# Optimization experiments

Measured on AMD Instinct MI355X. Metric: run time of the kernel, lower is better.

The kernel has to match this reference:

```python
import jax, jax.numpy as jnp
import numpy as np

EPS = 1e-8
NUM_HEADS = 8


def _conv(x, w, pad_h, pad_w):
    # x: (B,C,H,W) NCHW; w: (O,I,kh,kw) OIHW
    return jax.lax.conv_general_dilated(
        x, w, window_strides=(1, 1),
        padding=((pad_h, pad_h), (pad_w, pad_w)),
        dimension_numbers=('NCHW', 'OIHW', 'NCHW'))


def _mc_layernorm(x, g, b):
    # normalize over the features axis (axis=2) with per-(channel,feature) affine
    mu = jnp.mean(x, axis=2, keepdims=True)
    var = jnp.var(x, axis=2, keepdims=True)
    xn = (x - mu) * jax.lax.rsqrt(var + EPS)
    return xn * g[None, :, :, None] + b[None, :, :, None]


def _mc_attention(x, mem, wq, wk, wv, wo, prev_qk):
    # x: (B,C,F,W); projections are Conv2d with kernel (1,3), padding (0,1)
    B, _, F, W = x.shape
    q = _conv(x, wq, 0, 1)
    k = _conv(mem, wk, 0, 1)
    v = _conv(mem, wv, 0, 1)
    OC = q.shape[1]
    d = F // NUM_HEADS

    def split(t):  # (B,OC,F,W) -> (B,OC,heads,W,d)
        return t.reshape(B, OC, NUM_HEADS, d, W).transpose(0, 1, 2, 4, 3)

    q, k, v = split(q), split(k), split(v)
    qk = jnp.einsum('bchqd,bchkd->bchqk', q, k) / jnp.sqrt(jnp.asarray(d, x.dtype))
    if prev_qk is not None:
        qk = qk + prev_qk  # cross-layer additive qk bias accumulation
    a = jnp.einsum('bchqk,bchkd->bchqd', jax.nn.softmax(qk, axis=-1), v)
    a = a.transpose(0, 1, 2, 4, 3).reshape(B, OC, F, W)
    return _conv(a, wo, 0, 1), qk


def setup_inputs() -> dict:
    key = jax.random.key(0)
    ks = jax.random.split(key, 24)
    B, C, OC, F, W, H, EXP = 1, 8, 8, 1024, 512, NUM_HEADS, 4
    s = lambda fan: 1.0 / np.sqrt(fan)
    inp = {
        'x': jax.random.normal(ks[0], (B, C, F, W), jnp.float32),
        'skip': jax.random.normal(ks[1], (B, C, F, W), jnp.float32),
        'prev_qk1': jax.random.normal(ks[2], (B, OC, H, W, W), jnp.float32) * 0.5,
        'prev_qk2': jax.random.normal(ks[3], (B, OC, H, W, W), jnp.float32) * 0.5,
        'skip_qk': jax.random.normal(ks[4], (B, OC, H, W, W), jnp.float32) * 0.5,
        # norm1 / attn1 (self-attention on C channels -> OC)
        'g1': jnp.ones((C, F), jnp.float32),
        'b1': jnp.zeros((C, F), jnp.float32),
        'wq1': jax.random.normal(ks[5], (OC, C, 1, 3), jnp.float32) * s(C * 3),
        'wk1': jax.random.normal(ks[6], (OC, C, 1, 3), jnp.float32) * s(C * 3),
        'wv1': jax.random.normal(ks[7], (OC, C, 1, 3), jnp.float32) * s(C * 3),
        'wo1': jax.random.normal(ks[8], (OC, OC, 1, 3), jnp.float32) * s(OC * 3),
        # norm2 / attn2 (query from C+OC channels, memory = skip with C channels)
        'g2': jnp.ones((C + OC, F), jnp.float32),
        'b2': jnp.zeros((C + OC, F), jnp.float32),
        'wq2': jax.random.normal(ks[9], (OC, C + OC, 1, 3), jnp.float32) * s((C + OC) * 3),
        'wk2': jax.random.normal(ks[10], (OC, C, 1, 3), jnp.float32) * s(C * 3),
        'wv2': jax.random.normal(ks[11], (OC, C, 1, 3), jnp.float32) * s(C * 3),
        'wo2': jax.random.normal(ks[12], (OC, OC, 1, 3), jnp.float32) * s(OC * 3),
        # norm3 / conv MLP
        'g3': jnp.ones((C + 2 * OC, F), jnp.float32),
        'b3': jnp.zeros((C + 2 * OC, F), jnp.float32),
        'wc1': jax.random.normal(ks[13], (C * EXP, C + 2 * OC, 3, 3), jnp.float32) * s((C + 2 * OC) * 9),
        'wc2': jax.random.normal(ks[14], (C, C * EXP, 3, 3), jnp.float32) * s(C * EXP * 9),
    }
    return inp


def reference(x, skip, prev_qk1, prev_qk2, skip_qk,
              g1, b1, wq1, wk1, wv1, wo1,
              g2, b2, wq2, wk2, wv2, wo2,
              g3, b3, wc1, wc2):
    pq1 = prev_qk1 + skip_qk
    nx = _mc_layernorm(x, g1, b1)
    z, pq1 = _mc_attention(nx, nx, wq1, wk1, wv1, wo1, pq1)
    h = jnp.concatenate([x, z], axis=1)
    pq2 = skip_qk + pq1 + prev_qk2
    nh = _mc_layernorm(h, g2, b2)
    z, pq2 = _mc_attention(nh, skip, wq2, wk2, wv2, wo2, pq2)
    h = jnp.concatenate([h, z], axis=1)
    t = _conv(_mc_layernorm(h, g3, b3), wc1, 1, 1)
    t = jnp.square(jax.nn.relu(t))  # SquaredReLU
    z = _conv(t, wc2, 1, 1)
    # dropout is identity in eval mode
    return (x + z, pq1, pq2)
```

## Files before the change

kernel.cpp:

```cpp
#include <hip/hip_runtime.h>
#include <hip/hip_bf16.h>

#define F    1024
#define WW   512
#define DH   128
#define NPAIR 64
#define PW   514
#define PF   1026

using short8  = __attribute__((ext_vector_type(8))) short;
using short4v = __attribute__((ext_vector_type(4))) short;
using float4v = __attribute__((ext_vector_type(4))) float;

__device__ __forceinline__ float bf2f(unsigned short u) {
    union { unsigned int i; float f; } x; x.i = ((unsigned int)u) << 16; return x.f;
}
__device__ __forceinline__ unsigned short f2bf(float f) {
    union { float f; unsigned int i; } x; x.f = f;
    unsigned int r = x.i + 0x7fff + ((x.i >> 16) & 1);
    return (unsigned short)(r >> 16);
}

__global__ __launch_bounds__(256) void k_ln(
    const float* __restrict__ s0, const float* __restrict__ s1,
    const float* __restrict__ s2,
    const float* __restrict__ g, const float* __restrict__ b,
    unsigned short* __restrict__ out)
{
    int c  = blockIdx.x >> 5;
    int w0 = (blockIdx.x & 31) << 4;
    const float* src = (c < 8) ? s0 : (c < 16) ? s1 : s2;
    src += (size_t)(c & 7) * F * WW;
    int tx = threadIdx.x & 15, ty = threadIdx.x >> 4;

    float sum = 0.f, ssq = 0.f;
    for (int f = ty; f < F; f += 16) {
        float v = src[f * WW + w0 + tx];
        sum += v; ssq += v * v;
    }
    __shared__ float sm[16][17], sq[16][17];
    __shared__ float mu_s[16], rs_s[16];
    sm[ty][tx] = sum; sq[ty][tx] = ssq;
    __syncthreads();
    if (threadIdx.x < 16) {
        float s = 0.f, q = 0.f;
        #pragma unroll
        for (int i = 0; i < 16; i++) { s += sm[i][threadIdx.x]; q += sq[i][threadIdx.x]; }
        float mu  = s * (1.f / F);
        float var = q * (1.f / F) - mu * mu;
        mu_s[threadIdx.x] = mu;
        rs_s[threadIdx.x] = rsqrtf(var + 1e-8f);
    }
    __syncthreads();
    float mu = mu_s[tx], rs = rs_s[tx];
    unsigned short* o = out + (size_t)c * F * WW;
    for (int f = ty; f < F; f += 16) {
        float v = src[f * WW + w0 + tx];
        float r = (v - mu) * rs * g[c * F + f] + b[c * F + f];
        o[f * WW + w0 + tx] = f2bf(r);
    }
}

__global__ __launch_bounds__(256) void k_ln3_stats(
    const float* __restrict__ s0, const float* __restrict__ s1,
    const float* __restrict__ s2,
    float* __restrict__ mu3, float* __restrict__ rs3)
{
    int c  = blockIdx.x >> 5;
    int w0 = (blockIdx.x & 31) << 4;
    const float* src = (c < 8) ? s0 : (c < 16) ? s1 : s2;
    src += (size_t)(c & 7) * F * WW;
    int tx = threadIdx.x & 15, ty = threadIdx.x >> 4;

    float sum = 0.f, ssq = 0.f;
    for (int f = ty; f < F; f += 16) {
        float v = src[f * WW + w0 + tx];
        sum += v; ssq += v * v;
    }
    __shared__ float sm[16][17], sq[16][17];
    sm[ty][tx] = sum; sq[ty][tx] = ssq;
    __syncthreads();
    if (threadIdx.x < 16) {
        float s = 0.f, q = 0.f;
        #pragma unroll
        for (int i = 0; i < 16; i++) { s += sm[i][threadIdx.x]; q += sq[i][threadIdx.x]; }
        float mu  = s * (1.f / F);
        float var = q * (1.f / F) - mu * mu;
        mu3[c * WW + w0 + threadIdx.x] = mu;
        rs3[c * WW + w0 + threadIdx.x] = rsqrtf(var + 1e-8f);
    }
}

__global__ __launch_bounds__(256) void k_ln3_apply(
    const float* __restrict__ s0, const float* __restrict__ s1,
    const float* __restrict__ s2,
    const float* __restrict__ mu3, const float* __restrict__ rs3,
    const float* __restrict__ g, const float* __restrict__ b,
    unsigned short* __restrict__ outp)
{
    int p = blockIdx.x * 256 + threadIdx.x;
    int f = p >> 9, w = p & 511;
    unsigned short buf[32];
    #pragma unroll
    for (int c = 0; c < 24; c++) {
        const float* src = (c < 8) ? s0 : (c < 16) ? s1 : s2;
        float v = src[((size_t)(c & 7) * F + f) * WW + w];
        float r = (v - mu3[c * WW + w]) * rs3[c * WW + w] * g[c * F + f] + b[c * F + f];
        buf[c] = f2bf(r);
    }
    #pragma unroll
    for (int c = 24; c < 32; c++) buf[c] = 0;
    unsigned short* op = outp + ((size_t)(f + 1) * PW + (w + 1)) * 32;
    #pragma unroll
    for (int q = 0; q < 4; q++) *(short8*)(op + q * 8) = *(const short8*)(buf + q * 8);
}

__global__ void k_pad(unsigned short* __restrict__ a, unsigned short* __restrict__ b)
{
    int i = blockIdx.x * 256 + threadIdx.x;
    if (i >= 3076) return;
    int f, w;
    if (i < 514)       { f = 0;    w = i; }
    else if (i < 1028) { f = 1025; w = i - 514; }
    else { int j = i - 1028; f = 1 + (j >> 1); w = (j & 1) ? 513 : 0; }
    size_t off = ((size_t)f * PW + w) * 32;
    short8 z = {};
    #pragma unroll
    for (int q = 0; q < 4; q++) {
        *(short8*)(a + off + q * 8) = z;
        *(short8*)(b + off + q * 8) = z;
    }
}

__global__ void k_prep(const float* __restrict__ wc1, const float* __restrict__ wc2,
                       unsigned short* __restrict__ A1, unsigned short* __restrict__ A2)
{
    int i = blockIdx.x * 256 + threadIdx.x;
    if (i < 9216) {
        int ic = i & 31, row = i >> 5;
        int o16 = row & 15, tm = row >> 4;
        int tap = tm >> 1, m = tm & 1;
        int oc = m * 16 + o16;
        A1[i] = (ic < 24) ? f2bf(wc1[(oc * 24 + ic) * 9 + tap]) : (unsigned short)0;
    }
    if (i < 4608) {
        int ic = i & 31, row = i >> 5;
        int o = row & 15, tap = row >> 4;
        A2[i] = (o < 8) ? f2bf(wc2[(o * 32 + ic) * 9 + tap]) : (unsigned short)0;
    }
}

__global__ __launch_bounds__(256) void k_conv1m(
    const unsigned short* __restrict__ inp, const unsigned short* __restrict__ A1,
    unsigned short* __restrict__ outp)
{
    int wv = threadIdx.x >> 6, lane = threadIdx.x & 63;
    int lr = lane & 15, lkg = lane >> 4;

    short8 a[9][2];
    #pragma unroll
    for (int tap = 0; tap < 9; tap++)
        #pragma unroll
        for (int m = 0; m < 2; m++)
            a[tap][m] = *(const short8*)(A1 + ((tap * 2 + m) * 16 + lr) * 32 + lkg * 8);

    int f = blockIdx.x >> 1;
    int half = blockIdx.x & 1;
    for (int it = 0; it < 4; it++) {
        int w0 = (half * 16 + wv * 4 + it) * 16;
        float4v acc0 = {}, acc1 = {};
        #pragma unroll
        for (int dy = 0; dy < 3; dy++)
            #pragma unroll
            for (int dx = 0; dx < 3; dx++) {
                short8 bfrag = *(const short8*)(inp +
                    ((size_t)(f + dy) * PW + (w0 + lr + dx)) * 32 + lkg * 8);
                acc0 = __builtin_amdgcn_mfma_f32_16x16x32_bf16(a[dy*3+dx][0], bfrag, acc0, 0, 0, 0);
                acc1 = __builtin_amdgcn_mfma_f32_16x16x32_bf16(a[dy*3+dx][1], bfrag, acc1, 0, 0, 0);
            }
        unsigned short* op = outp + ((size_t)(f + 1) * PW + (w0 + lr + 1)) * 32;
        short4v o0, o1;
        #pragma unroll
        for (int r = 0; r < 4; r++) {
            float v0 = fmaxf(acc0[r], 0.f);
            float v1 = fmaxf(acc1[r], 0.f);
            o0[r] = (short)f2bf(v0 * v0);
            o1[r] = (short)f2bf(v1 * v1);
        }
        *(short4v*)(op + lkg * 4)      = o0;
        *(short4v*)(op + 16 + lkg * 4) = o1;
    }
}

__global__ __launch_bounds__(256) void k_conv2m(
    const unsigned short* __restrict__ inp, const unsigned short* __restrict__ A2,
    const float* __restrict__ x, float* __restrict__ out)
{
    int wv = threadIdx.x >> 6, lane = threadIdx.x & 63;
    int lr = lane & 15, lkg = lane >> 4;

    short8 a[9];
    #pragma unroll
    for (int tap = 0; tap < 9; tap++)
        a[tap] = *(const short8*)(A2 + (tap * 16 + lr) * 32 + lkg * 8);

    int f = blockIdx.x >> 1;
    int half = blockIdx.x & 1;
    for (int it = 0; it < 4; it++) {
        int w0 = (half * 16 + wv * 4 + it) * 16;
        float4v acc = {};
        #pragma unroll
        for (int dy = 0; dy < 3; dy++)
            #pragma unroll
            for (int dx = 0; dx < 3; dx++) {
                short8 bfrag = *(const short8*)(inp +
                    ((size_t)(f + dy) * PW + (w0 + lr + dx)) * 32 + lkg * 8);
                acc = __builtin_amdgcn_mfma_f32_16x16x32_bf16(a[dy*3+dx], bfrag, acc, 0, 0, 0);
            }
        if (lkg < 2) {
            #pragma unroll
            for (int r = 0; r < 4; r++) {
                int oc = lkg * 4 + r;
                size_t off = ((size_t)oc * F + f) * WW + w0 + lr;
                out[off] = x[off] + acc[r];
            }
        }
    }
}

__global__ __launch_bounds__(256) void k_qkv(
    const unsigned short* __restrict__ srcQ, int CinQ, const float* __restrict__ wq,
    const void* __restrict__ srcKV, int kvBf16,
    const float* __restrict__ wk, const float* __restrict__ wv,
    unsigned short* __restrict__ qT, unsigned short* __restrict__ kT,
    unsigned short* __restrict__ v)
{
    int vb = ((blockIdx.x & 31) << 4) + (blockIdx.x >> 5);
    int p0 = (vb * 256 + threadIdx.x) * 4;
    int f  = p0 >> 9;
    int w0 = p0 & 511;
    int h = f >> 7, jf = f & 127;

    float accq[8][4];
    #pragma unroll
    for (int o = 0; o < 8; o++) { accq[o][0]=0.f; accq[o][1]=0.f; accq[o][2]=0.f; accq[o][3]=0.f; }
    for (int ic = 0; ic < CinQ; ic++) {
        const unsigned short* s = srcQ + ((size_t)ic * F + f) * WW;
        float val[6];
        #pragma unroll
        for (int i = 0; i < 6; i++) {
            int w = w0 - 1 + i;
            val[i] = (w >= 0 && w < WW) ? bf2f(s[w]) : 0.f;
        }
        #pragma unroll
        for (int o = 0; o < 8; o++)
            #pragma unroll
            for (int t = 0; t < 3; t++) {
                float wt = wq[(o * CinQ + ic) * 3 + t];
                #pragma unroll
                for (int p = 0; p < 4; p++) accq[o][p] = fmaf(wt, val[p + t], accq[o][p]);
            }
    }
    #pragma unroll
    for (int o = 0; o < 8; o++)
        #pragma unroll
        for (int p = 0; p < 4; p++)
            qT[((size_t)(o * 8 + h) * WW + w0 + p) * DH + jf] = f2bf(accq[o][p]);

    float acck[8][4], accv[8][4];
    #pragma unroll
    for (int o = 0; o < 8; o++)
        #pragma unroll
        for (int p = 0; p < 4; p++) { acck[o][p] = 0.f; accv[o][p] = 0.f; }
    for (int ic = 0; ic < 8; ic++) {
        float val[6];
        if (kvBf16) {
            const unsigned short* s = (const unsigned short*)srcKV + ((size_t)ic * F + f) * WW;
            #pragma unroll
            for (int i = 0; i < 6; i++) {
                int w = w0 - 1 + i;
                val[i] = (w >= 0 && w < WW) ? bf2f(s[w]) : 0.f;
            }
        } else {
            const float* s = (const float*)srcKV + ((size_t)ic * F + f) * WW;
            #pragma unroll
            for (int i = 0; i < 6; i++) {
                int w = w0 - 1 + i;
                val[i] = (w >= 0 && w < WW) ? s[w] : 0.f;
            }
        }
        #pragma unroll
        for (int o = 0; o < 8; o++)
            #pragma unroll
            for (int t = 0; t < 3; t++) {
                float wtk = wk[(o * 8 + ic) * 3 + t];
                float wtv = wv[(o * 8 + ic) * 3 + t];
                #pragma unroll
                for (int p = 0; p < 4; p++) {
                    acck[o][p] = fmaf(wtk, val[p + t], acck[o][p]);
                    accv[o][p] = fmaf(wtv, val[p + t], accv[o][p]);
                }
            }
    }
    #pragma unroll
    for (int o = 0; o < 8; o++) {
        #pragma unroll
        for (int p = 0; p < 4; p++)
            kT[((size_t)(o * 8 + h) * WW + w0 + p) * DH + jf] = f2bf(acck[o][p]);
        short4v pv;
        #pragma unroll
        for (int p = 0; p < 4; p++) pv[p] = (short)f2bf(accv[o][p]);
        *(short4v*)(v + ((size_t)o * F + f) * WW + w0) = pv;
    }
}

__global__ __launch_bounds__(256) void k_attn(
    const unsigned short* __restrict__ qT, const unsigned short* __restrict__ kT,
    const unsigned short* __restrict__ v,
    const float* __restrict__ a0, const float* __restrict__ a1,
    const float* __restrict__ a2, int nsrc,
    float* __restrict__ pq, unsigned short* __restrict__ aout)
{
    int pair = blockIdx.x & 63;
    int qw0  = (blockIdx.x >> 6) << 6;

    __shared__ unsigned short Ks[64 * 136];
    __shared__ unsigned short Vt[128 * 72];
    __shared__ unsigned short P [64 * 72];

    int tid = threadIdx.x;
    const unsigned short* qb = qT + ((size_t)pair * WW + qw0) * DH;
    const unsigned short* kb = kT + (size_t)pair * WW * DH;
    const unsigned short* vb = v  + (size_t)pair * DH * WW;

    int wv = tid >> 6, lane = tid & 63;
    int lr = lane & 15, lkg = lane >> 4;
    int qrow = qw0 + wv * 16 + lr;

    short8 bq[4];
    #pragma unroll
    for (int dk = 0; dk < 4; dk++)
        bq[dk] = *(const short8*)(qb + (size_t)(wv * 16 + lr) * DH + dk * 32 + lkg * 8);

    float4v acc[8] = {};
    float mrun = -1e30f, lrun = 0.f;
    const float scale = 0.08838834764831845f;
    size_t bbase = (size_t)pair * WW * WW + (size_t)qrow * WW;

    for (int kc = 0; kc < 8; kc++) {
        __syncthreads();

        float4v b0v[4], b1v[4], b2v[4];
        #pragma unroll
        for (int mi = 0; mi < 4; mi++)
            b0v[mi] = *(const float4v*)(a0 + bbase + kc * 64 + mi * 16 + lkg * 4);
        if (nsrc > 1) {
            #pragma unroll
            for (int mi = 0; mi < 4; mi++)
                b1v[mi] = *(const float4v*)(a1 + bbase + kc * 64 + mi * 16 + lkg * 4);
        }
        if (nsrc > 2) {
            #pragma unroll
            for (int mi = 0; mi < 4; mi++)
                b2v[mi] = *(const float4v*)(a2 + bbase + kc * 64 + mi * 16 + lkg * 4);
        }

        #pragma unroll
        for (int it = 0; it < 4; it++) {
            int idx = it * 256 + tid;
            int r = idx >> 4, c = idx & 15;
            *(short8*)(Ks + r * 136 + c * 8) =
                *(const short8*)(kb + (size_t)(kc * 64 + r) * DH + c * 8);
        }
        #pragma unroll
        for (int it = 0; it < 4; it++) {
            int idx = it * 256 + tid;
            int j = idx >> 3, c = idx & 7;
            *(short8*)(Vt + j * 72 + c * 8) =
                *(const short8*)(vb + (size_t)j * WW + kc * 64 + c * 8);
        }
        __syncthreads();

        float4v sacc[4] = {};
        #pragma unroll
        for (int dk = 0; dk < 4; dk++) {
            short8 ak[4];
            #pragma unroll
            for (int mi = 0; mi < 4; mi++)
                ak[mi] = *(const short8*)(Ks + (mi * 16 + lr) * 136 + dk * 32 + lkg * 8);
            #pragma unroll
            for (int mi = 0; mi < 4; mi++)
                sacc[mi] = __builtin_amdgcn_mfma_f32_16x16x32_bf16(ak[mi], bq[dk], sacc[mi], 0, 0, 0);
        }

        float sv[4][4];
        float mx = -1e30f;
        #pragma unroll
        for (int mi = 0; mi < 4; mi++) {
            int k0 = kc * 64 + mi * 16 + lkg * 4;
            float4v s;
            #pragma unroll
            for (int r = 0; r < 4; r++) s[r] = sacc[mi][r] * scale + b0v[mi][r];
            if (nsrc > 1) {
                #pragma unroll
                for (int r = 0; r < 4; r++) s[r] += b1v[mi][r];
            }
            if (nsrc > 2) {
                #pragma unroll
                for (int r = 0; r < 4; r++) s[r] += b2v[mi][r];
            }
            *(float4v*)(pq + bbase + k0) = s;
            #pragma unroll
            for (int r = 0; r < 4; r++) { sv[mi][r] = s[r]; mx = fmaxf(mx, s[r]); }
        }
        mx = fmaxf(mx, __shfl_xor(mx, 16));
        mx = fmaxf(mx, __shfl_xor(mx, 32));
        float mnew  = fmaxf(mrun, mx);
        float alpha = __expf(mrun - mnew);
        float lsum  = 0.f;
        #pragma unroll
        for (int mi = 0; mi < 4; mi++) {
            short4v pk;
            #pragma unroll
            for (int r = 0; r < 4; r++) {
                float e = __expf(sv[mi][r] - mnew);
                lsum += e;
                pk[r] = (short)f2bf(e);
            }
            *(short4v*)(P + (wv * 16 + lr) * 72 + mi * 16 + lkg * 4) = pk;
        }
        lsum += __shfl_xor(lsum, 16);
        lsum += __shfl_xor(lsum, 32);
        lrun = lrun * alpha + lsum;
        mrun = mnew;

        #pragma unroll
        for (int mt = 0; mt < 8; mt++)
            #pragma unroll
            for (int r = 0; r < 4; r++) acc[mt][r] *= alpha;

        #pragma unroll
        for (int ks = 0; ks < 2; ks++) {
            short8 bp = *(const short8*)(P + (wv * 16 + lr) * 72 + ks * 32 + lkg * 8);
            #pragma unroll
            for (int mt = 0; mt < 8; mt++) {
                short8 av = *(const short8*)(Vt + (mt * 16 + lr) * 72 + ks * 32 + lkg * 8);
                acc[mt] = __builtin_amdgcn_mfma_f32_16x16x32_bf16(av, bp, acc[mt], 0, 0, 0);
            }
        }
    }

    float linv = 1.f / lrun;
    unsigned short* ab = aout + (size_t)pair * DH * WW + qw0 + wv * 16 + lr;
    #pragma unroll
    for (int mt = 0; mt < 8; mt++)
        #pragma unroll
        for (int r = 0; r < 4; r++) {
            int d = mt * 16 + lkg * 4 + r;
            ab[(size_t)d * WW] = f2bf(acc[mt][r] * linv);
        }
}

__global__ __launch_bounds__(256) void k_wo(
    const unsigned short* __restrict__ a, const float* __restrict__ w,
    float* __restrict__ z)
{
    int p0 = (blockIdx.x * 256 + threadIdx.x) * 4;
    int f = p0 >> 9, w0 = p0 & 511;
    float acc[8][4];
    #pragma unroll
    for (int o = 0; o < 8; o++)
        #pragma unroll
        for (int p = 0; p < 4; p++) acc[o][p] = 0.f;
    for (int ic = 0; ic < 8; ic++) {
        const unsigned short* s = a + ((size_t)ic * F + f) * WW;
        float val[6];
        #pragma unroll
        for (int i = 0; i < 6; i++) {
            int ww = w0 - 1 + i;
            val[i] = (ww >= 0 && ww < WW) ? bf2f(s[ww]) : 0.f;
        }
        #pragma unroll
        for (int o = 0; o < 8; o++)
            #pragma unroll
            for (int t = 0; t < 3; t++) {
                float wt = w[(o * 8 + ic) * 3 + t];
                #pragma unroll
                for (int p = 0; p < 4; p++) acc[o][p] = fmaf(wt, val[p + t], acc[o][p]);
            }
    }
    #pragma unroll
    for (int o = 0; o < 8; o++) {
        float4v ov;
        #pragma unroll
        for (int p = 0; p < 4; p++) ov[p] = acc[o][p];
        *(float4v*)(z + ((size_t)o * F + f) * WW + w0) = ov;
    }
}

extern "C" void kernel_launch(void* const* d_in, const int* in_sizes, int n_in,
                              void* d_out, int out_size, void* d_ws, size_t ws_size,
                              hipStream_t stream) {
    const float* x        = (const float*)d_in[0];
    const float* skip     = (const float*)d_in[1];
    const float* prev_qk1 = (const float*)d_in[2];
    const float* prev_qk2 = (const float*)d_in[3];
    const float* skip_qk  = (const float*)d_in[4];
    const float* g1  = (const float*)d_in[5];
    const float* b1  = (const float*)d_in[6];
    const float* wq1 = (const float*)d_in[7];
    const float* wk1 = (const float*)d_in[8];
    const float* wv1 = (const float*)d_in[9];
    const float* wo1 = (const float*)d_in[10];
    const float* g2  = (const float*)d_in[11];
    const float* b2  = (const float*)d_in[12];
    const float* wq2 = (const float*)d_in[13];
    const float* wk2 = (const float*)d_in[14];
    const float* wv2 = (const float*)d_in[15];
    const float* wo2 = (const float*)d_in[16];
    const float* g3  = (const float*)d_in[17];
    const float* b3  = (const float*)d_in[18];
    const float* wc1 = (const float*)d_in[19];
    const float* wc2 = (const float*)d_in[20];

    char* ws = (char*)d_ws;
    float*          z1 = (float*)(ws + 0);
    float*          z2 = (float*)(ws + 16777216);
    unsigned short* qT = (unsigned short*)(ws + 33554432);
    unsigned short* kT = (unsigned short*)(ws + 41943040);
    unsigned short* vB = (unsigned short*)(ws + 50331648);
    unsigned short* nh = (unsigned short*)(ws + 58720256);
    unsigned short* aB = (unsigned short*)(ws + 75497472);
    unsigned short* nh3p = (unsigned short*)(ws + 33554432);
    unsigned short* tBp  = (unsigned short*)(ws + 67305728);
    unsigned short* A1p  = (unsigned short*)(ws + 101057024);
    unsigned short* A2p  = (unsigned short*)(ws + 101075456);
    float*          mu3  = (float*)(ws + 101084672);
    float*          rs3  = (float*)(ws + 101133824);

    float* out0 = (float*)d_out;
    float* pq1  = out0 + 4194304;
    float* pq2  = pq1 + 16777216;

    k_prep<<<36, 256, 0, stream>>>(wc1, wc2, A1p, A2p);

    k_ln  <<<8 * 32,  256, 0, stream>>>(x, nullptr, nullptr, g1, b1, nh);
    k_qkv <<<512,     256, 0, stream>>>(nh, 8, wq1, nh, 1, wk1, wv1, qT, kT, vB);
    k_attn<<<512,     256, 0, stream>>>(qT, kT, vB, prev_qk1, skip_qk, nullptr, 2, pq1, aB);
    k_wo  <<<512,     256, 0, stream>>>(aB, wo1, z1);

    k_ln  <<<16 * 32, 256, 0, stream>>>(x, z1, nullptr, g2, b2, nh);
    k_qkv <<<512,     256, 0, stream>>>(nh, 16, wq2, skip, 0, wk2, wv2, qT, kT, vB);
    k_attn<<<512,     256, 0, stream>>>(qT, kT, vB, skip_qk, pq1, prev_qk2, 3, pq2, aB);
    k_wo  <<<512,     256, 0, stream>>>(aB, wo2, z2);

    k_pad      <<<13,      256, 0, stream>>>(nh3p, tBp);
    k_ln3_stats<<<24 * 32, 256, 0, stream>>>(x, z1, z2, mu3, rs3);
    k_ln3_apply<<<2048,    256, 0, stream>>>(x, z1, z2, mu3, rs3, g3, b3, nh3p);
    k_conv1m   <<<2048,    256, 0, stream>>>(nh3p, A1p, tBp);
    k_conv2m   <<<2048,    256, 0, stream>>>(tBp, A2p, x, out0);
}
```

Measured before the change: 771.1 us.

## Stage Q/K transposes through LDS and prefetch K/V tiles in registers in attention

In k_qkv the blocks are retiled into 32x32 (f,w) tiles and the transposed Q and K outputs are staged through a shared-memory buffer. This turns scattered 2-byte stores into contiguous 16-byte stores. In k_attn the next K/V chunk is loaded into registers while the current chunk is being computed, with setprio around the MFMA sections and a launch bound of 2 blocks. The prefetch raises register pressure, and the qkv kernel's launch geometry must match the new 16-blocks-per-f-row mapping.

Result: faster. 673.2 us (-12.7%).

```diff
diff --git a/kernel.cpp b/kernel.cpp
--- a/kernel.cpp
+++ b/kernel.cpp
@@ -235,11 +235,14 @@
     unsigned short* __restrict__ qT, unsigned short* __restrict__ kT,
     unsigned short* __restrict__ v)
 {
-    int vb = ((blockIdx.x & 31) << 4) + (blockIdx.x >> 5);
-    int p0 = (vb * 256 + threadIdx.x) * 4;
-    int f  = p0 >> 9;
-    int w0 = p0 & 511;
-    int h = f >> 7, jf = f & 127;
+    int bf = blockIdx.x >> 4, bw = blockIdx.x & 15;
+    int f0 = bf << 5, w0t = bw << 5;
+    int fy = threadIdx.x >> 3, wx = threadIdx.x & 7;
+    int f  = f0 + fy;
+    int w0 = w0t + (wx << 2);
+    int h  = f0 >> 7, jf0 = f0 & 127;
+
+    __shared__ unsigned short T[8][32][33];
 
     float accq[8][4];
     #pragma unroll
@@ -265,7 +268,7 @@
     for (int o = 0; o < 8; o++)
         #pragma unroll
         for (int p = 0; p < 4; p++)
-            qT[((size_t)(o * 8 + h) * WW + w0 + p) * DH + jf] = f2bf(accq[o][p]);
+            T[o][(wx << 2) + p][fy] = f2bf(accq[o][p]);
 
     float acck[8][4], accv[8][4];
     #pragma unroll
@@ -304,17 +307,41 @@
     }
     #pragma unroll
     for (int o = 0; o < 8; o++) {
+        short4v tv;
+        #pragma unroll
+        for (int p = 0; p < 4; p++) tv[p] = (short)f2bf(accv[o][p]);
+        *(short4v*)(v + ((size_t)o * F + f) * WW + w0) = tv;
+    }
+
+    __syncthreads();
+    #pragma unroll
+    for (int it = 0; it < 4; it++) {
+        int u = it * 256 + threadIdx.x;
+        int jq = u & 3, w = (u >> 2) & 31, o = u >> 7;
+        short8 vv;
+        #pragma unroll
+        for (int i = 0; i < 8; i++) vv[i] = (short)T[o][w][jq * 8 + i];
+        *(short8*)(qT + ((size_t)((o << 3) + h) * WW + w0t + w) * DH + jf0 + (jq << 3)) = vv;
+    }
+    __syncthreads();
+    #pragma unroll
+    for (int o = 0; o < 8; o++)
         #pragma unroll
         for (int p = 0; p < 4; p++)
-            kT[((size_t)(o * 8 + h) * WW + w0 + p) * DH + jf] = f2bf(acck[o][p]);
-        short4v pv;
-        #pragma unroll
-        for (int p = 0; p < 4; p++) pv[p] = (short)f2bf(accv[o][p]);
-        *(short4v*)(v + ((size_t)o * F + f) * WW + w0) = pv;
-    }
-}
-
-__global__ __launch_bounds__(256) void k_attn(
+            T[o][(wx << 2) + p][fy] = f2bf(acck[o][p]);
+    __syncthreads();
+    #pragma unroll
+    for (int it = 0; it < 4; it++) {
+        int u = it * 256 + threadIdx.x;
+        int jq = u & 3, w = (u >> 2) & 31, o = u >> 7;
+        short8 vv;
+        #pragma unroll
+        for (int i = 0; i < 8; i++) vv[i] = (short)T[o][w][jq * 8 + i];
+        *(short8*)(kT + ((size_t)((o << 3) + h) * WW + w0t + w) * DH + jf0 + (jq << 3)) = vv;
+    }
+}
+
+__global__ __launch_bounds__(256, 2) void k_attn(
     const unsigned short* __restrict__ qT, const unsigned short* __restrict__ kT,
     const unsigned short* __restrict__ v,
     const float* __restrict__ a0, const float* __restrict__ a1,
@@ -342,14 +369,41 @@
     for (int dk = 0; dk < 4; dk++)
         bq[dk] = *(const short8*)(qb + (size_t)(wv * 16 + lr) * DH + dk * 32 + lkg * 8);
 
+    #pragma unroll
+    for (int it = 0; it < 4; it++) {
+        int idx = it * 256 + tid;
+        int r = idx >> 4, c = idx & 15;
+        *(short8*)(Ks + r * 136 + c * 8) = *(const short8*)(kb + (size_t)r * DH + c * 8);
+    }
+    #pragma unroll
+    for (int it = 0; it < 4; it++) {
+        int idx = it * 256 + tid;
+        int j = idx >> 3, c = idx & 7;
+        *(short8*)(Vt + j * 72 + c * 8) = *(const short8*)(vb + (size_t)j * WW + c * 8);
+    }
+    __syncthreads();
+
     float4v acc[8] = {};
     float mrun = -1e30f, lrun = 0.f;
     const float scale = 0.08838834764831845f;
     size_t bbase = (size_t)pair * WW * WW + (size_t)qrow * WW;
 
     for (int kc = 0; kc < 8; kc++) {
-        __syncthreads();
-
+        short8 krx[4], vrx[4];
+        if (kc < 7) {
+            #pragma unroll
+            for (int it = 0; it < 4; it++) {
+                int idx = it * 256 + tid;
+                int r = idx >> 4, c = idx & 15;
+                krx[it] = *(const short8*)(kb + (size_t)((kc + 1) * 64 + r) * DH + c * 8);
+            }
+            #pragma unroll
+            for (int it = 0; it < 4; it++) {
+                int idx = it * 256 + tid;
+                int j = idx >> 3, c = idx & 7;
+                vrx[it] = *(const short8*)(vb + (size_t)j * WW + (kc + 1) * 64 + c * 8);
+            }
+        }
         float4v b0v[4], b1v[4], b2v[4];
         #pragma unroll
         for (int mi = 0; mi < 4; mi++)
@@ -365,23 +419,8 @@
                 b2v[mi] = *(const float4v*)(a2 + bbase + kc * 64 + mi * 16 + lkg * 4);
         }
 
-        #pragma unroll
-        for (int it = 0; it < 4; it++) {
-            int idx = it * 256 + tid;
-            int r = idx >> 4, c = idx & 15;
-            *(short8*)(Ks + r * 136 + c * 8) =
-                *(const short8*)(kb + (size_t)(kc * 64 + r) * DH + c * 8);
-        }
-        #pragma unroll
-        for (int it = 0; it < 4; it++) {
-            int idx = it * 256 + tid;
-            int j = idx >> 3, c = idx & 7;
-            *(short8*)(Vt + j * 72 + c * 8) =
-                *(const short8*)(vb + (size_t)j * WW + kc * 64 + c * 8);
-        }
-        __syncthreads();
-
         float4v sacc[4] = {};
+        __builtin_amdgcn_s_setprio(1);
         #pragma unroll
         for (int dk = 0; dk < 4; dk++) {
             short8 ak[4];
@@ -392,6 +431,7 @@
             for (int mi = 0; mi < 4; mi++)
                 sacc[mi] = __builtin_amdgcn_mfma_f32_16x16x32_bf16(ak[mi], bq[dk], sacc[mi], 0, 0, 0);
         }
+        __builtin_amdgcn_s_setprio(0);
 
         float sv[4][4];
         float mx = -1e30f;
@@ -439,6 +479,7 @@
             #pragma unroll
             for (int r = 0; r < 4; r++) acc[mt][r] *= alpha;
 
+        __builtin_amdgcn_s_setprio(1);
         #pragma unroll
         for (int ks = 0; ks < 2; ks++) {
             short8 bp = *(const short8*)(P + (wv * 16 + lr) * 72 + ks * 32 + lkg * 8);
@@ -448,6 +489,24 @@
                 acc[mt] = __builtin_amdgcn_mfma_f32_16x16x32_bf16(av, bp, acc[mt], 0, 0, 0);
             }
         }
+        __builtin_amdgcn_s_setprio(0);
+
+        __syncthreads();
+        if (kc < 7) {
+            #pragma unroll
+            for (int it = 0; it < 4; it++) {
+                int idx = it * 256 + tid;
+                int r = idx >> 4, c = idx & 15;
+                *(short8*)(Ks + r * 136 + c * 8) = krx[it];
+            }
+            #pragma unroll
+            for (int it = 0; it < 4; it++) {
+                int idx = it * 256 + tid;
+                int j = idx >> 3, c = idx & 7;
+                *(short8*)(Vt + j * 72 + c * 8) = vrx[it];
+            }
+        }
+        __syncthreads();
     }
 
     float linv = 1.f / lrun;
```
